# Performance work log

Hardware: AMD Instinct MI355X
Metric: run time of the kernel (lower is better)

The kernel has to match this reference:

```python
import jax, jax.numpy as jnp
import numpy as np

B, C, H, W = 16, 64, 256, 256
WF = W // 2 + 1  # rfft last-dim size = 129


def setup_inputs() -> dict:
    key = jax.random.key(0)
    k1, k2, k3 = jax.random.split(key, 3)
    x = jax.random.normal(k1, (B, C, H, W), dtype=jnp.float32)
    # He-style complex init scale: 1/sqrt(fan_in)/4 (Rayleigh modulus); use scaled normals for determinism
    s = 1.0 / np.sqrt(C) / 4.0
    w_real = jax.random.normal(k2, (1, C, H, WF), dtype=jnp.float32) * s
    w_imag = jax.random.normal(k3, (1, C, H, WF), dtype=jnp.float32) * s
    return {"x": x, "w_real": w_real, "w_imag": w_imag}


def reference(x, w_real, w_imag):
    # 2D rFFT over (H, W)  -> complex [B, C, H, W//2+1]
    xf = jnp.fft.rfftn(x, axes=(-2, -1))
    xr, xi = xf.real, xf.imag
    # complex elementwise multiply with per-channel spectral weights
    yr = xr * w_real - xi * w_imag
    yi = xr * w_imag + xi * w_real
    y = jax.lax.complex(yr, yi)
    # inverse rFFT back to [B, C, H, W]; stride == 1, so no subsampling
    return jnp.fft.irfftn(y, s=(H, W), axes=(-2, -1))
```

## Files before the change

### kernel.cpp

```cpp
#include <hip/hip_runtime.h>


#define PHYS(i) ((i) + ((i) >> 4))

typedef float fvec4 __attribute__((ext_vector_type(4)));

__device__ __forceinline__ float4 nt_load4(const float* p) {
    fvec4 v = __builtin_nontemporal_load((const fvec4*)p);
    return make_float4(v.x, v.y, v.z, v.w);
}
__device__ __forceinline__ void nt_store4(float* p, float4 v) {
    fvec4 t;
    t.x = v.x; t.y = v.y; t.z = v.z; t.w = v.w;
    __builtin_nontemporal_store(t, (fvec4*)p);
}

__device__ __forceinline__ float2 cmulf(float2 a, float2 b) {
    return make_float2(fmaf(a.x, b.x, -a.y * b.y), fmaf(a.x, b.y, a.y * b.x));
}

__device__ __forceinline__ void wave_sync() {
    asm volatile("s_waitcnt lgkmcnt(0)" ::: "memory");
    __builtin_amdgcn_wave_barrier();
}

struct Tw {
    float2 a1, a2, a3;
    float2 b1, b2, b3;
    float2 c1, c2, c3;
};

__device__ __forceinline__ void tw_one(int lane, int Ns, float2& w1, float2& w2, float2& w3) {
    int r = lane & (Ns - 1);
    float th = -6.283185307179586f * (float)r / (float)(4 * Ns);
    float s1, c1;
    __sincosf(th, &s1, &c1);
    w1 = make_float2(c1, s1);
    w2 = make_float2(c1 * c1 - s1 * s1, 2.0f * c1 * s1);
    w3 = make_float2(w2.x * c1 - w2.y * s1, w2.y * c1 + w2.x * s1);
}

__device__ __forceinline__ Tw make_tw(int lane) {
    Tw t;
    tw_one(lane, 4,  t.a1, t.a2, t.a3);
    tw_one(lane, 16, t.b1, t.b2, t.b3);
    tw_one(lane, 64, t.c1, t.c2, t.c3);
    return t;
}

template<int NS, int DIR>
__device__ __forceinline__ void stage(const float2* s, float2* d, int j,
                                      float2 w1, float2 w2, float2 w3)
{
    float2 v0 = s[PHYS(j)];
    float2 v1 = s[PHYS(j + 64)];
    float2 v2 = s[PHYS(j + 128)];
    float2 v3 = s[PHYS(j + 192)];
    if (NS > 1) {
        v1 = cmulf(v1, w1);
        v2 = cmulf(v2, w2);
        v3 = cmulf(v3, w3);
    }
    float t0x = v0.x + v2.x, t0y = v0.y + v2.y;
    float t1x = v0.x - v2.x, t1y = v0.y - v2.y;
    float t2x = v1.x + v3.x, t2y = v1.y + v3.y;
    float t3x = v1.x - v3.x, t3y = v1.y - v3.y;
    float ix = (DIR < 0) ? t3y : -t3y;
    float iy = (DIR < 0) ? -t3x : t3x;
    int r = j & (NS - 1);
    int base = ((j & ~(NS - 1)) << 2) | r;
    d[PHYS(base)]          = make_float2(t0x + t2x, t0y + t2y);
    d[PHYS(base + NS)]     = make_float2(t1x + ix, t1y + iy);
    d[PHYS(base + 2*NS)]   = make_float2(t0x - t2x, t0y - t2y);
    d[PHYS(base + 3*NS)]   = make_float2(t1x - ix, t1y - iy);
}

template<int DIR>
__device__ __forceinline__ void fft256(float2* b0, float2* b1, int lane, const Tw& t)
{
    const float sg = (DIR < 0) ? 1.0f : -1.0f;
    float2 a1 = make_float2(t.a1.x, sg * t.a1.y), a2 = make_float2(t.a2.x, sg * t.a2.y),
           a3 = make_float2(t.a3.x, sg * t.a3.y);
    float2 bb1 = make_float2(t.b1.x, sg * t.b1.y), bb2 = make_float2(t.b2.x, sg * t.b2.y),
           bb3 = make_float2(t.b3.x, sg * t.b3.y);
    float2 cc1 = make_float2(t.c1.x, sg * t.c1.y), cc2 = make_float2(t.c2.x, sg * t.c2.y),
           cc3 = make_float2(t.c3.x, sg * t.c3.y);
    wave_sync();
    stage<1,  DIR>(b0, b1, lane, a1, a1, a1);
    wave_sync();
    stage<4,  DIR>(b1, b0, lane, a1, a2, a3);
    wave_sync();
    stage<16, DIR>(b0, b1, lane, bb1, bb2, bb3);
    wave_sync();
    stage<64, DIR>(b1, b0, lane, cc1, cc2, cc3);
    wave_sync();
}

__global__ __launch_bounds__(256) void k_wt(const float* __restrict__ wre,
                                            const float* __restrict__ wim,
                                            float2* __restrict__ wt)
{
    __shared__ float tr[32 * 129];
    __shared__ float ti[32 * 129];
    const int c  = blockIdx.x >> 3;
    const int h0 = (blockIdx.x & 7) * 32;
    const float* pr = wre + ((size_t)c * 256 + h0) * 129;
    const float* pi = wim + ((size_t)c * 256 + h0) * 129;
    for (int idx = threadIdx.x; idx < 32 * 129; idx += 256) {
        tr[idx] = pr[idx];
        ti[idx] = pi[idx];
    }
    __syncthreads();
    for (int idx = threadIdx.x; idx < 129 * 32; idx += 256) {
        int wf = idx >> 5, hl = idx & 31;
        wt[((size_t)c * 129 + wf) * 256 + h0 + hl] =
            make_float2(tr[hl * 129 + wf], ti[hl * 129 + wf]);
    }
}

__global__ __launch_bounds__(256) void k_rows_fwd(const float* __restrict__ x,
                                                  float* __restrict__ ws)
{
    __shared__ float2 buf[2][4][272];
    const int lane = threadIdx.x & 63;
    const int wv   = threadIdx.x >> 6;
    const int rp   = blockIdx.x * 4 + wv;
    const float* srcA = x + (size_t)rp * 512;
    const float* srcB = srcA + 256;

    Tw tw = make_tw(lane);

    float4 av = nt_load4(srcA + lane * 4);
    float4 bv = nt_load4(srcB + lane * 4);
    float2* B0 = buf[0][wv];
    float2* B1 = buf[1][wv];
    B0[PHYS(4*lane + 0)] = make_float2(av.x, bv.x);
    B0[PHYS(4*lane + 1)] = make_float2(av.y, bv.y);
    B0[PHYS(4*lane + 2)] = make_float2(av.z, bv.z);
    B0[PHYS(4*lane + 3)] = make_float2(av.w, bv.w);

    fft256<-1>(B0, B1, lane, tw);

    const float2* F = B0;
    float4 oa, ob;
    if (lane == 0) {
        float2 Z0 = F[PHYS(0)], Z128 = F[PHYS(128)];
        float2 Z1 = F[PHYS(1)], Zm = F[PHYS(255)];
        float2 A1 = make_float2(0.5f * (Z1.x + Zm.x), 0.5f * (Z1.y - Zm.y));
        float2 Bd = make_float2(0.5f * (Z1.x - Zm.x), 0.5f * (Z1.y + Zm.y));
        float2 B1f = make_float2(Bd.y, -Bd.x);
        oa = make_float4(Z0.x, Z128.x, A1.x, A1.y);
        ob = make_float4(Z0.y, Z128.y, B1f.x, B1f.y);
    } else {
        int k0 = 2 * lane;
        float2 Zk0 = F[PHYS(k0)],     Zm0 = F[PHYS(256 - k0)];
        float2 Zk1 = F[PHYS(k0 + 1)], Zm1 = F[PHYS(255 - k0)];
        float2 A0 = make_float2(0.5f * (Zk0.x + Zm0.x), 0.5f * (Zk0.y - Zm0.y));
        float2 D0 = make_float2(0.5f * (Zk0.x - Zm0.x), 0.5f * (Zk0.y + Zm0.y));
        float2 Bf0 = make_float2(D0.y, -D0.x);
        float2 A1 = make_float2(0.5f * (Zk1.x + Zm1.x), 0.5f * (Zk1.y - Zm1.y));
        float2 D1 = make_float2(0.5f * (Zk1.x - Zm1.x), 0.5f * (Zk1.y + Zm1.y));
        float2 Bf1 = make_float2(D1.y, -D1.x);
        oa = make_float4(A0.x, A0.y, A1.x, A1.y);
        ob = make_float4(Bf0.x, Bf0.y, Bf1.x, Bf1.y);
    }
    float* dstA = ws + (size_t)rp * 512;
    *(float4*)(dstA + lane * 4)       = oa;
    *(float4*)(dstA + 256 + lane * 4) = ob;
}

template<bool USEWT>
__global__ __launch_bounds__(512) void k_cols(float* __restrict__ ws,
                                              const float* __restrict__ wre,
                                              const float* __restrict__ wim,
                                              const float2* __restrict__ wt)
{
    __shared__ float2 buf[2][8][272];
    const int tid  = threadIdx.x;
    const int lane = tid & 63;
    const int wv   = tid >> 6;
    const int nwg  = gridDim.x;
    const int L    = (blockIdx.x & 7) * (nwg >> 3) + (blockIdx.x >> 3);
    const int grp  = L & 15;
    const int img  = L >> 4;
    const int c    = img & 63;
    const int p0   = grp * 8;
    const int pair = p0 + wv;
    float* base = ws + (size_t)img * 65536;

    Tw tw = make_tw(lane);

    const int cbase = c * 256;
    float2 pw[4];
    if (USEWT) {
        const float2* wp = wt + ((size_t)c * 129 + pair) * 256;
#pragma unroll
        for (int t = 0; t < 4; ++t) pw[t] = wp[lane + 64 * t];
    } else {
#pragma unroll
        for (int t = 0; t < 4; ++t) {
            int ik = (cbase + lane + 64 * t) * 129 + pair;
            pw[t] = make_float2(wre[ik], wim[ik]);
        }
    }

    for (int q = tid; q < 1024; q += 512) {
        int h = q >> 2, j4 = q & 3;
        float4 v = *(const float4*)(base + h * 256 + p0 * 2 + j4 * 4);
        buf[0][2*j4    ][PHYS(h)] = make_float2(v.x, v.y);
        buf[0][2*j4 + 1][PHYS(h)] = make_float2(v.z, v.w);
    }
    __syncthreads();

    float2* B0 = buf[0][wv];
    float2* B1 = buf[1][wv];
    fft256<-1>(B0, B1, lane, tw);

    const float g = 1.0f / 65536.0f;
    {
        const float2* S = B0;
        float2* D = B1;
        if (pair == 0) {
#pragma unroll
            for (int t = 0; t < 4; ++t) {
                int k = lane + 64 * t;
                int m = (256 - k) & 255;
                float2 Sk = S[PHYS(k)], Sm = S[PHYS(m)];
                float2 S0   = make_float2(0.5f * (Sk.x + Sm.x), 0.5f * (Sk.y - Sm.y));
                float2 Dk   = make_float2(0.5f * (Sk.x - Sm.x), 0.5f * (Sk.y + Sm.y));
                float2 S128 = make_float2(Dk.y, -Dk.x);
                float2 wk0, wm0, wk128, wm128;
                if (USEWT) {
                    const float2* w0row   = wt + ((size_t)c * 129 +   0) * 256;
                    const float2* w128row = wt + ((size_t)c * 129 + 128) * 256;
                    wk0 = w0row[k];  wm0 = w0row[m];
                    wk128 = w128row[k];  wm128 = w128row[m];
                } else {
                    int ik = (cbase + k) * 129, im = (cbase + m) * 129;
                    wk0   = make_float2(wre[ik], wim[ik]);
                    wm0   = make_float2(wre[im], wim[im]);
                    wk128 = make_float2(wre[ik + 128], wim[ik + 128]);
                    wm128 = make_float2(wre[im + 128], wim[im + 128]);
                }
                float2 A0   = make_float2(0.5f * g * (wk0.x + wm0.x),
                                          0.5f * g * (wk0.y - wm0.y));
                float2 A128 = make_float2(0.5f * g * (wk128.x + wm128.x),
                                          0.5f * g * (wk128.y - wm128.y));
                float2 y0 = cmulf(S0, A0);
                float2 y1 = cmulf(S128, A128);
                D[PHYS(k)] = make_float2(y0.x - y1.y, y0.y + y1.x);
            }
        } else {
#pragma unroll
            for (int t = 0; t < 4; ++t) {
                int k = lane + 64 * t;
                float2 Sk = S[PHYS(k)];
                float2 W = make_float2(g * pw[t].x, g * pw[t].y);
                D[PHYS(k)] = cmulf(Sk, W);
            }
        }
    }
    fft256<+1>(B1, B0, lane, tw);

    __syncthreads();
    for (int q = tid; q < 1024; q += 512) {
        int h = q >> 2, j4 = q & 3;
        float2 a = buf[1][2*j4    ][PHYS(h)];
        float2 b = buf[1][2*j4 + 1][PHYS(h)];
        *(float4*)(base + h * 256 + p0 * 2 + j4 * 4) = make_float4(a.x, a.y, b.x, b.y);
    }
}

__global__ __launch_bounds__(256) void k_rows_inv(float* __restrict__ ws)
{
    __shared__ float2 buf[2][4][272];
    const int lane = threadIdx.x & 63;
    const int wv   = threadIdx.x >> 6;
    const int rp   = blockIdx.x * 4 + wv;
    float* rowA = ws + (size_t)rp * 512;
    float* rowB = rowA + 256;

    Tw tw = make_tw(lane);

    float4 va = *(const float4*)(rowA + lane * 4);
    float4 vb = *(const float4*)(rowB + lane * 4);
    float2* B0 = buf[0][wv];
    float2* B1 = buf[1][wv];
    if (lane == 0) {
        B0[PHYS(0)]   = make_float2(va.x, vb.x);
        B0[PHYS(128)] = make_float2(va.y, vb.y);
        B0[PHYS(1)]   = make_float2(va.z - vb.w, va.w + vb.z);
        B0[PHYS(255)] = make_float2(va.z + vb.w, -va.w + vb.z);
    } else {
        int k0 = 2 * lane;
        B0[PHYS(k0)]        = make_float2(va.x - vb.y, va.y + vb.x);
        B0[PHYS(256 - k0)]  = make_float2(va.x + vb.y, -va.y + vb.x);
        B0[PHYS(k0 + 1)]    = make_float2(va.z - vb.w, va.w + vb.z);
        B0[PHYS(255 - k0)]  = make_float2(va.z + vb.w, -va.w + vb.z);
    }

    fft256<+1>(B0, B1, lane, tw);

    const float2* F = B0;
    float2 f0 = F[PHYS(4*lane)], f1 = F[PHYS(4*lane + 1)];
    float2 f2 = F[PHYS(4*lane + 2)], f3 = F[PHYS(4*lane + 3)];
    nt_store4(rowA + lane * 4, make_float4(f0.x, f1.x, f2.x, f3.x));
    nt_store4(rowB + lane * 4, make_float4(f0.y, f1.y, f2.y, f3.y));
}

extern "C" void kernel_launch(void* const* d_in, const int* in_sizes, int n_in,
                              void* d_out, int out_size, void* d_ws, size_t ws_size,
                              hipStream_t stream)
{
    (void)in_sizes; (void)n_in; (void)out_size;
    const float* x   = (const float*)d_in[0];
    const float* wre = (const float*)d_in[1];
    const float* wim = (const float*)d_in[2];
    float* out = (float*)d_out;
    float2* wt = (float2*)d_ws;

    const size_t wt_bytes = (size_t)64 * 129 * 256 * sizeof(float2);
    const bool use_wt = (ws_size >= wt_bytes);

    if (use_wt) {
        k_wt<<<dim3(512), dim3(256), 0, stream>>>(wre, wim, wt);
    }
    k_rows_fwd<<<dim3(32768), dim3(256), 0, stream>>>(x, out);
    if (use_wt)
        k_cols<true ><<<dim3(16384), dim3(512), 0, stream>>>(out, wre, wim, wt);
    else
        k_cols<false><<<dim3(16384), dim3(512), 0, stream>>>(out, wre, wim, wt);
    k_rows_inv<<<dim3(32768), dim3(256), 0, stream>>>(out);
}
```

Before: 692.0 us.

## Rewrite column FFT as register-resident 16x16 decomposition with 16 lanes per column

The column pass now gives each 256-point column to 16 threads. Each thread holds 16 values in registers and runs two radix-16 DFTs with one shared-memory transpose in between, instead of four radix-4 stages that round-trip through LDS. Each block now covers 16 column pairs with 256 threads. Separately, the padded LDS index is replaced with an XOR swizzle, which shrinks the row buffers. The intent is fewer LDS passes and syncs and more arithmetic per load, at the cost of higher register pressure.

```diff
diff --git a/kernel.cpp b/kernel.cpp
--- a/kernel.cpp
+++ b/kernel.cpp
@@ -1,7 +1,7 @@
 #include <hip/hip_runtime.h>
 
 
-#define PHYS(i) ((i) + ((i) >> 4))
+#define PHX(i) ((i) ^ ((i) >> 2))
 
 typedef float fvec4 __attribute__((ext_vector_type(4)));
 
@@ -18,11 +18,93 @@
 __device__ __forceinline__ float2 cmulf(float2 a, float2 b) {
     return make_float2(fmaf(a.x, b.x, -a.y * b.y), fmaf(a.x, b.y, a.y * b.x));
 }
+__device__ __forceinline__ float2 cadd(float2 a, float2 b){ return make_float2(a.x+b.x, a.y+b.y); }
+__device__ __forceinline__ float2 csub(float2 a, float2 b){ return make_float2(a.x-b.x, a.y-b.y); }
+__device__ __forceinline__ float2 mulmi(float2 a){ return make_float2(a.y, -a.x); }
+__device__ __forceinline__ float2 mulpi(float2 a){ return make_float2(-a.y, a.x); }
 
 __device__ __forceinline__ void wave_sync() {
     asm volatile("s_waitcnt lgkmcnt(0)" ::: "memory");
     __builtin_amdgcn_wave_barrier();
 }
+
+
+template<int DIR>
+__device__ __forceinline__ void dft4(float2 x0, float2 x1, float2 x2, float2 x3,
+                                     float2& y0, float2& y1, float2& y2, float2& y3)
+{
+    float2 s0 = cadd(x0, x2), d0 = csub(x0, x2);
+    float2 s1 = cadd(x1, x3), d1 = csub(x1, x3);
+    y0 = cadd(s0, s1);
+    y2 = csub(s0, s1);
+    float2 jd1 = (DIR < 0) ? mulmi(d1) : mulpi(d1);
+    y1 = cadd(d0, jd1);
+    y3 = csub(d0, jd1);
+}
+
+template<int DIR>
+__device__ __forceinline__ float2 twd(float2 a, float wr, float wi) {
+    return cmulf(a, make_float2(wr, (DIR < 0) ? wi : -wi));
+}
+
+template<int DIR>
+__device__ __forceinline__ void dft16(float2 v[16])
+{
+    const float C1 = 0.92387953251128674f;
+    const float S1 = 0.38268343236508978f;
+    const float R  = 0.70710678118654752f;
+    float2 a0, a1, a2, a3;
+    dft4<DIR>(v[0], v[4], v[8],  v[12], a0, a1, a2, a3);
+    float2 u00 = a0, u01 = a1, u02 = a2, u03 = a3;
+    dft4<DIR>(v[1], v[5], v[9],  v[13], a0, a1, a2, a3);
+    float2 u10 = a0;
+    float2 u11 = twd<DIR>(a1,  C1, -S1);
+    float2 u12 = twd<DIR>(a2,   R,  -R);
+    float2 u13 = twd<DIR>(a3,  S1, -C1);
+    dft4<DIR>(v[2], v[6], v[10], v[14], a0, a1, a2, a3);
+    float2 u20 = a0;
+    float2 u21 = twd<DIR>(a1,   R,  -R);
+    float2 u22 = (DIR < 0) ? mulmi(a2) : mulpi(a2);
+    float2 u23 = twd<DIR>(a3,  -R,  -R);
+    dft4<DIR>(v[3], v[7], v[11], v[15], a0, a1, a2, a3);
+    float2 u30 = a0;
+    float2 u31 = twd<DIR>(a1,  S1, -C1);
+    float2 u32 = twd<DIR>(a2,  -R,  -R);
+    float2 u33 = twd<DIR>(a3, -C1,  S1);
+    dft4<DIR>(u00, u10, u20, u30, v[0], v[4], v[8],  v[12]);
+    dft4<DIR>(u01, u11, u21, u31, v[1], v[5], v[9],  v[13]);
+    dft4<DIR>(u02, u12, u22, u32, v[2], v[6], v[10], v[14]);
+    dft4<DIR>(u03, u13, u23, u33, v[3], v[7], v[11], v[15]);
+}
+
+template<int DIR>
+__device__ __forceinline__ void midtw(float2 v[16], int n2)
+{
+    float th = ((DIR < 0) ? -6.283185307179586f : 6.283185307179586f)
+               * (float)n2 * (1.0f / 256.0f);
+    float s, c;
+    __sincosf(th, &s, &c);
+    float2 base = make_float2(c, s);
+    float2 w = base;
+    v[1] = cmulf(v[1], w);
+#pragma unroll
+    for (int k = 2; k < 16; ++k) { w = cmulf(w, base); v[k] = cmulf(v[k], w); }
+}
+
+template<int DIR>
+__device__ __forceinline__ void gfft(float2 v[16], float2* Ag, int l)
+{
+    dft16<DIR>(v);
+    midtw<DIR>(v, l);
+    wave_sync();
+#pragma unroll
+    for (int k = 0; k < 16; ++k) Ag[l * 17 + k] = v[k];
+    wave_sync();
+#pragma unroll
+    for (int n = 0; n < 16; ++n) v[n] = Ag[n * 17 + l];
+    dft16<DIR>(v);
+}
+
 
 struct Tw {
     float2 a1, a2, a3;
@@ -52,10 +134,10 @@
 __device__ __forceinline__ void stage(const float2* s, float2* d, int j,
                                       float2 w1, float2 w2, float2 w3)
 {
-    float2 v0 = s[PHYS(j)];
-    float2 v1 = s[PHYS(j + 64)];
-    float2 v2 = s[PHYS(j + 128)];
-    float2 v3 = s[PHYS(j + 192)];
+    float2 v0 = s[PHX(j)];
+    float2 v1 = s[PHX(j + 64)];
+    float2 v2 = s[PHX(j + 128)];
+    float2 v3 = s[PHX(j + 192)];
     if (NS > 1) {
         v1 = cmulf(v1, w1);
         v2 = cmulf(v2, w2);
@@ -69,10 +151,10 @@
     float iy = (DIR < 0) ? -t3x : t3x;
     int r = j & (NS - 1);
     int base = ((j & ~(NS - 1)) << 2) | r;
-    d[PHYS(base)]          = make_float2(t0x + t2x, t0y + t2y);
-    d[PHYS(base + NS)]     = make_float2(t1x + ix, t1y + iy);
-    d[PHYS(base + 2*NS)]   = make_float2(t0x - t2x, t0y - t2y);
-    d[PHYS(base + 3*NS)]   = make_float2(t1x - ix, t1y - iy);
+    d[PHX(base)]          = make_float2(t0x + t2x, t0y + t2y);
+    d[PHX(base + NS)]     = make_float2(t1x + ix, t1y + iy);
+    d[PHX(base + 2*NS)]   = make_float2(t0x - t2x, t0y - t2y);
+    d[PHX(base + 3*NS)]   = make_float2(t1x - ix, t1y - iy);
 }
 
 template<int DIR>
@@ -121,7 +203,7 @@
 __global__ __launch_bounds__(256) void k_rows_fwd(const float* __restrict__ x,
                                                   float* __restrict__ ws)
 {
-    __shared__ float2 buf[2][4][272];
+    __shared__ float2 buf[2][4][256];
     const int lane = threadIdx.x & 63;
     const int wv   = threadIdx.x >> 6;
     const int rp   = blockIdx.x * 4 + wv;
@@ -134,18 +216,18 @@
     float4 bv = nt_load4(srcB + lane * 4);
     float2* B0 = buf[0][wv];
     float2* B1 = buf[1][wv];
-    B0[PHYS(4*lane + 0)] = make_float2(av.x, bv.x);
-    B0[PHYS(4*lane + 1)] = make_float2(av.y, bv.y);
-    B0[PHYS(4*lane + 2)] = make_float2(av.z, bv.z);
-    B0[PHYS(4*lane + 3)] = make_float2(av.w, bv.w);
+    B0[PHX(4*lane + 0)] = make_float2(av.x, bv.x);
+    B0[PHX(4*lane + 1)] = make_float2(av.y, bv.y);
+    B0[PHX(4*lane + 2)] = make_float2(av.z, bv.z);
+    B0[PHX(4*lane + 3)] = make_float2(av.w, bv.w);
 
     fft256<-1>(B0, B1, lane, tw);
 
     const float2* F = B0;
     float4 oa, ob;
     if (lane == 0) {
-        float2 Z0 = F[PHYS(0)], Z128 = F[PHYS(128)];
-        float2 Z1 = F[PHYS(1)], Zm = F[PHYS(255)];
+        float2 Z0 = F[PHX(0)], Z128 = F[PHX(128)];
+        float2 Z1 = F[PHX(1)], Zm = F[PHX(255)];
         float2 A1 = make_float2(0.5f * (Z1.x + Zm.x), 0.5f * (Z1.y - Zm.y));
         float2 Bd = make_float2(0.5f * (Z1.x - Zm.x), 0.5f * (Z1.y + Zm.y));
         float2 B1f = make_float2(Bd.y, -Bd.x);
@@ -153,8 +235,8 @@
         ob = make_float4(Z0.y, Z128.y, B1f.x, B1f.y);
     } else {
         int k0 = 2 * lane;
-        float2 Zk0 = F[PHYS(k0)],     Zm0 = F[PHYS(256 - k0)];
-        float2 Zk1 = F[PHYS(k0 + 1)], Zm1 = F[PHYS(255 - k0)];
+        float2 Zk0 = F[PHX(k0)],     Zm0 = F[PHX(256 - k0)];
+        float2 Zk1 = F[PHX(k0 + 1)], Zm1 = F[PHX(255 - k0)];
         float2 A0 = make_float2(0.5f * (Zk0.x + Zm0.x), 0.5f * (Zk0.y - Zm0.y));
         float2 D0 = make_float2(0.5f * (Zk0.x - Zm0.x), 0.5f * (Zk0.y + Zm0.y));
         float2 Bf0 = make_float2(D0.y, -D0.x);
@@ -170,110 +252,120 @@
 }
 
 template<bool USEWT>
-__global__ __launch_bounds__(512) void k_cols(float* __restrict__ ws,
-                                              const float* __restrict__ wre,
-                                              const float* __restrict__ wim,
-                                              const float2* __restrict__ wt)
-{
-    __shared__ float2 buf[2][8][272];
-    const int tid  = threadIdx.x;
-    const int lane = tid & 63;
-    const int wv   = tid >> 6;
-    const int nwg  = gridDim.x;
-    const int L    = (blockIdx.x & 7) * (nwg >> 3) + (blockIdx.x >> 3);
-    const int grp  = L & 15;
-    const int img  = L >> 4;
-    const int c    = img & 63;
-    const int p0   = grp * 8;
-    const int pair = p0 + wv;
+__global__ __launch_bounds__(256) void k_cols_r(float* __restrict__ ws,
+                                                const float2* __restrict__ wt,
+                                                const float* __restrict__ wre,
+                                                const float* __restrict__ wim)
+{
+    __shared__ float2 A[16][273];
+    const int tid = threadIdx.x;
+    const int l   = tid & 15;
+    const int gk  = tid >> 4;
+    const int nwg = gridDim.x;
+    const int Lb  = (blockIdx.x & 7) * (nwg >> 3) + (blockIdx.x >> 3);
+    const int pg  = Lb & 7;
+    const int img = Lb >> 3;
+    const int c   = img & 63;
+    const int p0  = pg * 16;
+    const int pair = p0 + gk;
     float* base = ws + (size_t)img * 65536;
-
-    Tw tw = make_tw(lane);
-
-    const int cbase = c * 256;
-    float2 pw[4];
+    float2* Ag = A[gk];
+    const float gn = 1.0f / 65536.0f;
+
+    float2 W[16];
     if (USEWT) {
         const float2* wp = wt + ((size_t)c * 129 + pair) * 256;
 #pragma unroll
-        for (int t = 0; t < 4; ++t) pw[t] = wp[lane + 64 * t];
+        for (int k2 = 0; k2 < 16; ++k2) W[k2] = wp[l + 16 * k2];
     } else {
 #pragma unroll
-        for (int t = 0; t < 4; ++t) {
-            int ik = (cbase + lane + 64 * t) * 129 + pair;
-            pw[t] = make_float2(wre[ik], wim[ik]);
+        for (int k2 = 0; k2 < 16; ++k2) {
+            int ik = (c * 256 + l + 16 * k2) * 129 + pair;
+            W[k2] = make_float2(wre[ik], wim[ik]);
         }
     }
 
-    for (int q = tid; q < 1024; q += 512) {
-        int h = q >> 2, j4 = q & 3;
-        float4 v = *(const float4*)(base + h * 256 + p0 * 2 + j4 * 4);
-        buf[0][2*j4    ][PHYS(h)] = make_float2(v.x, v.y);
-        buf[0][2*j4 + 1][PHYS(h)] = make_float2(v.z, v.w);
+#pragma unroll
+    for (int i = 0; i < 8; ++i) {
+        int idx = tid + 256 * i;
+        int h = idx >> 3, q = idx & 7;
+        float4 xv = *(const float4*)(base + h * 256 + p0 * 2 + q * 4);
+        A[2*q    ][h] = make_float2(xv.x, xv.y);
+        A[2*q + 1][h] = make_float2(xv.z, xv.w);
     }
     __syncthreads();
 
-    float2* B0 = buf[0][wv];
-    float2* B1 = buf[1][wv];
-    fft256<-1>(B0, B1, lane, tw);
-
-    const float g = 1.0f / 65536.0f;
-    {
-        const float2* S = B0;
-        float2* D = B1;
-        if (pair == 0) {
-#pragma unroll
-            for (int t = 0; t < 4; ++t) {
-                int k = lane + 64 * t;
-                int m = (256 - k) & 255;
-                float2 Sk = S[PHYS(k)], Sm = S[PHYS(m)];
-                float2 S0   = make_float2(0.5f * (Sk.x + Sm.x), 0.5f * (Sk.y - Sm.y));
-                float2 Dk   = make_float2(0.5f * (Sk.x - Sm.x), 0.5f * (Sk.y + Sm.y));
-                float2 S128 = make_float2(Dk.y, -Dk.x);
-                float2 wk0, wm0, wk128, wm128;
-                if (USEWT) {
-                    const float2* w0row   = wt + ((size_t)c * 129 +   0) * 256;
-                    const float2* w128row = wt + ((size_t)c * 129 + 128) * 256;
-                    wk0 = w0row[k];  wm0 = w0row[m];
-                    wk128 = w128row[k];  wm128 = w128row[m];
-                } else {
-                    int ik = (cbase + k) * 129, im = (cbase + m) * 129;
-                    wk0   = make_float2(wre[ik], wim[ik]);
-                    wm0   = make_float2(wre[im], wim[im]);
-                    wk128 = make_float2(wre[ik + 128], wim[ik + 128]);
-                    wm128 = make_float2(wre[im + 128], wim[im + 128]);
-                }
-                float2 A0   = make_float2(0.5f * g * (wk0.x + wm0.x),
-                                          0.5f * g * (wk0.y - wm0.y));
-                float2 A128 = make_float2(0.5f * g * (wk128.x + wm128.x),
-                                          0.5f * g * (wk128.y - wm128.y));
-                float2 y0 = cmulf(S0, A0);
-                float2 y1 = cmulf(S128, A128);
-                D[PHYS(k)] = make_float2(y0.x - y1.y, y0.y + y1.x);
+    float2 v[16];
+#pragma unroll
+    for (int n1 = 0; n1 < 16; ++n1) v[n1] = Ag[16 * n1 + l];
+
+    gfft<-1>(v, Ag, l);
+
+    if (pair == 0) {
+        wave_sync();
+#pragma unroll
+        for (int k2 = 0; k2 < 16; ++k2) Ag[l + 16 * k2] = v[k2];
+        wave_sync();
+        float2 sm[16];
+#pragma unroll
+        for (int k2 = 0; k2 < 16; ++k2) {
+            int m = (256 - (l + 16 * k2)) & 255;
+            sm[k2] = Ag[m];
+        }
+#pragma unroll
+        for (int k2 = 0; k2 < 16; ++k2) {
+            int k = l + 16 * k2;
+            int m = (256 - k) & 255;
+            float2 Sk = v[k2], Sm = sm[k2];
+            float2 S0   = make_float2(0.5f * (Sk.x + Sm.x), 0.5f * (Sk.y - Sm.y));
+            float2 Dk   = make_float2(0.5f * (Sk.x - Sm.x), 0.5f * (Sk.y + Sm.y));
+            float2 S128 = make_float2(Dk.y, -Dk.x);
+            float2 wk0, wm0, wk128, wm128;
+            if (USEWT) {
+                const float2* w0r   = wt + ((size_t)c * 129 +   0) * 256;
+                const float2* w128r = wt + ((size_t)c * 129 + 128) * 256;
+                wk0 = W[k2];  wm0 = w0r[m];
+                wk128 = w128r[k];  wm128 = w128r[m];
+            } else {
+                int ik = (c * 256 + k) * 129, im = (c * 256 + m) * 129;
+                wk0   = make_float2(wre[ik], wim[ik]);
+                wm0   = make_float2(wre[im], wim[im]);
+                wk128 = make_float2(wre[ik + 128], wim[ik + 128]);
+                wm128 = make_float2(wre[im + 128], wim[im + 128]);
             }
-        } else {
-#pragma unroll
-            for (int t = 0; t < 4; ++t) {
-                int k = lane + 64 * t;
-                float2 Sk = S[PHYS(k)];
-                float2 W = make_float2(g * pw[t].x, g * pw[t].y);
-                D[PHYS(k)] = cmulf(Sk, W);
-            }
+            float2 A0   = make_float2(0.5f * gn * (wk0.x + wm0.x),
+                                      0.5f * gn * (wk0.y - wm0.y));
+            float2 A128 = make_float2(0.5f * gn * (wk128.x + wm128.x),
+                                      0.5f * gn * (wk128.y - wm128.y));
+            float2 y0 = cmulf(S0, A0);
+            float2 y1 = cmulf(S128, A128);
+            v[k2] = make_float2(y0.x - y1.y, y0.y + y1.x);
         }
-    }
-    fft256<+1>(B1, B0, lane, tw);
-
+    } else {
+#pragma unroll
+        for (int k2 = 0; k2 < 16; ++k2)
+            v[k2] = cmulf(v[k2], make_float2(gn * W[k2].x, gn * W[k2].y));
+    }
+
+    gfft<+1>(v, Ag, l);
+
+    wave_sync();
+#pragma unroll
+    for (int k2 = 0; k2 < 16; ++k2) Ag[l + 16 * k2] = v[k2];
     __syncthreads();
-    for (int q = tid; q < 1024; q += 512) {
-        int h = q >> 2, j4 = q & 3;
-        float2 a = buf[1][2*j4    ][PHYS(h)];
-        float2 b = buf[1][2*j4 + 1][PHYS(h)];
-        *(float4*)(base + h * 256 + p0 * 2 + j4 * 4) = make_float4(a.x, a.y, b.x, b.y);
+#pragma unroll
+    for (int i = 0; i < 8; ++i) {
+        int idx = tid + 256 * i;
+        int h = idx >> 3, q = idx & 7;
+        float2 a = A[2*q    ][h];
+        float2 b = A[2*q + 1][h];
+        *(float4*)(base + h * 256 + p0 * 2 + q * 4) = make_float4(a.x, a.y, b.x, b.y);
     }
 }
 
 __global__ __launch_bounds__(256) void k_rows_inv(float* __restrict__ ws)
 {
-    __shared__ float2 buf[2][4][272];
+    __shared__ float2 buf[2][4][256];
     const int lane = threadIdx.x & 63;
     const int wv   = threadIdx.x >> 6;
     const int rp   = blockIdx.x * 4 + wv;
@@ -287,23 +379,23 @@
     float2* B0 = buf[0][wv];
     float2* B1 = buf[1][wv];
     if (lane == 0) {
-        B0[PHYS(0)]   = make_float2(va.x, vb.x);
-        B0[PHYS(128)] = make_float2(va.y, vb.y);
-        B0[PHYS(1)]   = make_float2(va.z - vb.w, va.w + vb.z);
-        B0[PHYS(255)] = make_float2(va.z + vb.w, -va.w + vb.z);
+        B0[PHX(0)]   = make_float2(va.x, vb.x);
+        B0[PHX(128)] = make_float2(va.y, vb.y);
+        B0[PHX(1)]   = make_float2(va.z - vb.w, va.w + vb.z);
+        B0[PHX(255)] = make_float2(va.z + vb.w, -va.w + vb.z);
     } else {
         int k0 = 2 * lane;
-        B0[PHYS(k0)]        = make_float2(va.x - vb.y, va.y + vb.x);
-        B0[PHYS(256 - k0)]  = make_float2(va.x + vb.y, -va.y + vb.x);
-        B0[PHYS(k0 + 1)]    = make_float2(va.z - vb.w, va.w + vb.z);
-        B0[PHYS(255 - k0)]  = make_float2(va.z + vb.w, -va.w + vb.z);
+        B0[PHX(k0)]        = make_float2(va.x - vb.y, va.y + vb.x);
+        B0[PHX(256 - k0)]  = make_float2(va.x + vb.y, -va.y + vb.x);
+        B0[PHX(k0 + 1)]    = make_float2(va.z - vb.w, va.w + vb.z);
+        B0[PHX(255 - k0)]  = make_float2(va.z + vb.w, -va.w + vb.z);
     }
 
     fft256<+1>(B0, B1, lane, tw);
 
     const float2* F = B0;
-    float2 f0 = F[PHYS(4*lane)], f1 = F[PHYS(4*lane + 1)];
-    float2 f2 = F[PHYS(4*lane + 2)], f3 = F[PHYS(4*lane + 3)];
+    float2 f0 = F[PHX(4*lane)], f1 = F[PHX(4*lane + 1)];
+    float2 f2 = F[PHX(4*lane + 2)], f3 = F[PHX(4*lane + 3)];
     nt_store4(rowA + lane * 4, make_float4(f0.x, f1.x, f2.x, f3.x));
     nt_store4(rowB + lane * 4, make_float4(f0.y, f1.y, f2.y, f3.y));
 }
@@ -327,8 +419,8 @@
     }
     k_rows_fwd<<<dim3(32768), dim3(256), 0, stream>>>(x, out);
     if (use_wt)
-        k_cols<true ><<<dim3(16384), dim3(512), 0, stream>>>(out, wre, wim, wt);
+        k_cols_r<true ><<<dim3(8192), dim3(256), 0, stream>>>(out, wt, wre, wim);
     else
-        k_cols<false><<<dim3(16384), dim3(512), 0, stream>>>(out, wre, wim, wt);
+        k_cols_r<false><<<dim3(8192), dim3(256), 0, stream>>>(out, wt, wre, wim);
     k_rows_inv<<<dim3(32768), dim3(256), 0, stream>>>(out);
 }
```

Result: faster. 632.1 us (-8.7%).
